# Optimization experiments

Hardware: AMD Instinct MI355X
Metric: run time of the kernel (lower is better)

Reference implementation:

```python
import jax, jax.numpy as jnp
import numpy as np

B, T, D, H = 8, 1024, 512, 8
HD = D // H  # head_dim = 64


def conv1d(x, w, b):
    # x: [B, C_in, T], w: [C_out, C_in, 3], 'same' padding
    y = jax.lax.conv_general_dilated(x, w, (1,), [(1, 1)],
                                     dimension_numbers=('NCH', 'OIH', 'NCH'))
    return y + b[None, :, None]


def setup_inputs() -> dict:
    key = jax.random.key(0)
    ks = jax.random.split(key, 9)
    s = 0.05
    return {
        'x': jax.random.normal(ks[0], (B, T, D), dtype=jnp.float32),
        'w11': jax.random.normal(ks[1], (D, D, 3), dtype=jnp.float32) * s,
        'b11': jnp.zeros((D,), dtype=jnp.float32),
        'w12': jax.random.normal(ks[2], (D, D, 3), dtype=jnp.float32) * s,
        'b12': jnp.zeros((D,), dtype=jnp.float32),
        'w13': jax.random.normal(ks[3], (D, D, 3), dtype=jnp.float32) * s,
        'b13': jnp.zeros((D,), dtype=jnp.float32),
        'w2': jax.random.normal(ks[4], (D, 2 * D, 3), dtype=jnp.float32) * s,
        'b2': jnp.zeros((D,), dtype=jnp.float32),
    }


def reference(x, w11, b11, w12, b12, w13, b13, w2, b2):
    # dropout is identity in eval mode
    b, t, d = x.shape
    xc = jnp.transpose(x, (0, 2, 1))  # [B, D, T]

    def proj(w, bb):
        y = jax.nn.relu(conv1d(xc, w, bb))        # [B, D, T]
        y = jnp.transpose(y, (0, 2, 1))           # [B, T, D]
        return y.reshape(b, t, H, HD)             # [B, T, H, HD]

    q = proj(w11, b11)
    k = proj(w12, b12)
    v = proj(w13, b13)

    # ---- time-wise attention (d_k = head_dim) ----
    qf = jnp.transpose(q, (0, 2, 1, 3))  # [B, H, T, HD]
    kf = jnp.transpose(k, (0, 2, 1, 3))
    vf = jnp.transpose(v, (0, 2, 1, 3))
    sf = jnp.einsum('bhtd,bhsd->bhts', qf, kf) / np.sqrt(HD)  # [B,H,T,T]
    af = jax.nn.softmax(sf, axis=-1)
    valuesf = jnp.einsum('bhts,bhsd->bhtd', af, vf)           # [B,H,T,HD]
    valuesf = jnp.transpose(valuesf, (0, 2, 1, 3)).reshape(b, t, H * HD)

    # ---- channel-wise attention (d_k = T, scores over head_dim) ----
    qt = jnp.transpose(q, (0, 2, 3, 1))  # [B, H, HD, T]
    kt = jnp.transpose(k, (0, 2, 3, 1))
    vt = jnp.transpose(v, (0, 2, 3, 1))
    st = jnp.einsum('bhct,bhdt->bhcd', qt, kt) / np.sqrt(t)   # [B,H,HD,HD]
    at = jax.nn.softmax(st, axis=-1)
    valuest = jnp.einsum('bhcd,bhdt->bhct', at, vt)           # [B,H,HD,T]
    # torch: permute(0,2,3,1).reshape(B, T, H*HD)
    valuest = jnp.transpose(valuest, (0, 2, 3, 1)).reshape(b, t, H * HD)

    values = jnp.concatenate([valuesf, valuest], axis=-1)     # [B, T, 2D]
    values = jnp.transpose(values, (0, 2, 1))                 # [B, 2D, T]
    out = jax.nn.relu(conv1d(values, w2, b2))                 # [B, D, T]
    return jnp.transpose(out, (0, 2, 1))                      # [B, T, D]
```

## Files before the change

kernel.cpp:

```cpp
#include <hip/hip_runtime.h>

#define BB 8
#define TT 1024
#define DD 512
#define DD2 1024
#define HH 8
#define HDIM 64
#define TP (TT + 2)

typedef short short8 __attribute__((ext_vector_type(8)));
typedef float floatx4 __attribute__((ext_vector_type(4)));

typedef const __attribute__((address_space(1))) unsigned int* gas_ptr;
typedef __attribute__((address_space(3))) unsigned int* las_ptr;

__device__ __forceinline__ unsigned short f2bf(float f) {
    union { float f; unsigned u; } v; v.f = f;
    unsigned r = v.u + 0x7fffu + ((v.u >> 16) & 1u);
    return (unsigned short)(r >> 16);
}

__device__ __forceinline__ void gl2lds16(const void* g, void* l) {
    __builtin_amdgcn_global_load_lds((gas_ptr)g, (las_ptr)l, 16, 0, 0);
}

__global__ void k_convert_x(const float* __restrict__ x, unsigned short* __restrict__ xp) {
    int idx = blockIdx.x * 256 + threadIdx.x;
    const int total = BB * TP * DD;
    if (idx >= total) return;
    int c = idx % DD;
    int rt = idx / DD;
    int row = rt % TP;
    int b = rt / TP;
    float v = 0.f;
    if (row >= 1 && row <= TT) v = x[(b * TT + row - 1) * DD + c];
    xp[idx] = f2bf(v);
}

__global__ void k_convert_wqkv(const float* __restrict__ w0, const float* __restrict__ w1,
                               const float* __restrict__ w2, unsigned short* __restrict__ out) {
    int idx = blockIdx.x * 256 + threadIdx.x;
    const int total = 9 << 18;
    if (idx >= total) return;
    int e = idx & 7;
    int lane = (idx >> 3) & 63;
    int co0 = (idx >> 9) & 31;
    int ci0 = (idx >> 14) & 15;
    int rest = idx >> 18;
    int k = rest % 3, p = rest / 3;
    int co = co0 * 16 + (lane & 15);
    int ci = ci0 * 32 + (lane >> 4) * 8 + e;
    const float* w = (p == 0) ? w0 : ((p == 1) ? w1 : w2);
    out[idx] = f2bf(w[(co * DD + ci) * 3 + k]);
}

__global__ void k_convert_w2(const float* __restrict__ w, unsigned short* __restrict__ out) {
    int idx = blockIdx.x * 256 + threadIdx.x;
    const int total = 3 << 19;
    if (idx >= total) return;
    int e = idx & 7;
    int lane = (idx >> 3) & 63;
    int co0 = (idx >> 9) & 31;
    int ci0 = (idx >> 14) & 31;
    int k = idx >> 19;
    int co = co0 * 16 + (lane & 15);
    int ci = ci0 * 32 + (lane >> 4) * 8 + e;
    out[idx] = f2bf(w[(co * DD2 + ci) * 3 + k]);
}

__global__ void k_zero_aux(unsigned short* __restrict__ vp, float* __restrict__ gbuf) {
    int idx = blockIdx.x * 256 + threadIdx.x;
    if (idx < BB * 2 * 2 * DD) {
        int c = idx % (2 * DD);
        int t1 = idx / (2 * DD);
        int row = (t1 & 1) ? (TT + 1) : 0;
        int b = t1 >> 1;
        vp[(b * TP + row) * (2 * DD) + c] = 0;
    }
    if (idx < 64 * HDIM * HDIM) gbuf[idx] = 0.f;
}

__global__ __launch_bounds__(256) void k_qkv_conv(
    const unsigned short* __restrict__ xp, const unsigned short* __restrict__ wfrag,
    const float* __restrict__ b11, const float* __restrict__ b12, const float* __restrict__ b13,
    unsigned short* __restrict__ q, unsigned short* __restrict__ qt,
    unsigned short* __restrict__ kfrag, unsigned short* __restrict__ kt,
    unsigned short* __restrict__ v, unsigned short* __restrict__ vtfrag) {
    __shared__ short As[2][144 * 32];
    int wave = threadIdx.x >> 6, lane = threadIdx.x & 63;
    int l15 = lane & 15, quad = lane >> 4;
    int wm = wave >> 1, wn = wave & 1;
    int tb = blockIdx.x * 128;
    int cb = blockIdx.y * 128;
    int proj = blockIdx.z % 3, b = blockIdx.z / 3;
    const short* A = (const short*)xp + b * TP * DD;
    const short* WF = (const short*)wfrag + (size_t)proj * 786432 + lane * 8;
    int srow = lane >> 2;
    int scs = (((lane & 3) ^ (srow & 3)) << 3);
    int co0b = (cb >> 4) + wn * 4;

    floatx4 acc[4][4];
#pragma unroll
    for (int mi = 0; mi < 4; ++mi)
#pragma unroll
        for (int ni = 0; ni < 4; ++ni) acc[mi][ni] = (floatx4){0.f, 0.f, 0.f, 0.f};

    for (int j = wave; j < 9; j += 4)
        gl2lds16(A + (tb + j * 16 + srow) * DD + scs, &As[0][j * 512]);
    __syncthreads();

    for (int it = 0; it < 16; ++it) {
        if (it < 15) {
            for (int j = wave; j < 9; j += 4)
                gl2lds16(A + (tb + j * 16 + srow) * DD + (it + 1) * 32 + scs,
                         &As[(it + 1) & 1][j * 512]);
        }
        const short* Asb = As[it & 1];
        short8 bf[3][4];
#pragma unroll
        for (int k = 0; k < 3; ++k)
#pragma unroll
            for (int ni = 0; ni < 4; ++ni)
                bf[k][ni] = *(const short8*)(WF + ((size_t)((k * 16 + it) * 32 + co0b + ni) << 9));
#pragma unroll
        for (int k = 0; k < 3; ++k) {
            short8 af[4];
#pragma unroll
            for (int mi = 0; mi < 4; ++mi) {
                int arow = wm * 64 + mi * 16 + l15 + k;
                af[mi] = *(const short8*)&Asb[arow * 32 + ((quad ^ (arow & 3)) << 3)];
            }
#pragma unroll
            for (int mi = 0; mi < 4; ++mi)
#pragma unroll
                for (int ni = 0; ni < 4; ++ni)
                    acc[mi][ni] = __builtin_amdgcn_mfma_f32_16x16x32_bf16(af[mi], bf[k][ni], acc[mi][ni], 0, 0, 0);
        }
        __syncthreads();
    }

    const float* bias = (proj == 0) ? b11 : ((proj == 1) ? b12 : b13);
#pragma unroll
    for (int ni = 0; ni < 4; ++ni) {
        int co = cb + wn * 64 + ni * 16 + l15;
        float bv = bias[co];
        int h = co >> 6, hd = co & 63;
        int bh = b * HH + h;
#pragma unroll
        for (int mi = 0; mi < 4; ++mi) {
            int tbase = tb + wm * 64 + mi * 16 + quad * 4;
            unsigned short bb[4];
            ushort4 pk;
#pragma unroll
            for (int r = 0; r < 4; ++r) {
                float val = fmaxf(acc[mi][ni][r] + bv, 0.f);
                bb[r] = f2bf(val);
                ((unsigned short*)&pk)[r] = bb[r];
            }
            if (proj == 0) {
#pragma unroll
                for (int r = 0; r < 4; ++r)
                    q[((size_t)bh * TT + tbase + r) * HDIM + hd] = bb[r];
                *(ushort4*)&qt[((size_t)bh * HDIM + hd) * TT + tbase] = pk;
            } else if (proj == 1) {
                *(ushort4*)&kt[((size_t)bh * HDIM + hd) * TT + tbase] = pk;
                int sblk = tbase >> 6;
                int jr = (quad & 1) + 2 * (mi >> 1);
                int l15a_base = 4 * (quad >> 1) + 8 * (mi & 1);
                int kf = hd >> 5, quad_a = (hd >> 3) & 3, elem = hd & 7;
                size_t base = ((((size_t)bh * 16 + sblk) * 4 + jr) * 2 + kf) * 512 +
                              quad_a * 128 + elem;
#pragma unroll
                for (int r = 0; r < 4; ++r)
                    kfrag[base + (l15a_base + r) * 8] = bb[r];
            } else {
#pragma unroll
                for (int r = 0; r < 4; ++r)
                    v[((size_t)bh * TT + tbase + r) * HDIM + hd] = bb[r];
                int sblk = tbase >> 6;
                int df = hd >> 4, l15a = hd & 15;
                int kf = mi >> 1;
                int quad_a = 2 * (mi & 1) + (quad >> 1);
                int elem = (quad & 1) * 4;
                size_t base = ((((size_t)bh * 16 + sblk) * 4 + df) * 2 + kf) * 512 +
                              (quad_a * 16 + l15a) * 8 + elem;
                *(ushort4*)&vtfrag[base] = pk;
            }
        }
    }
}

__global__ __launch_bounds__(256) void k_time_attn(
    const unsigned short* __restrict__ q, const unsigned short* __restrict__ kfrag,
    const unsigned short* __restrict__ vtfrag, unsigned short* __restrict__ vp) {
    int wave = threadIdx.x >> 6, lane = threadIdx.x & 63;
    int l15 = lane & 15, quad = lane >> 4;
    int bh = blockIdx.y;
    int b = bh >> 3, h = bh & 7;
    int qr = blockIdx.x * 64 + wave * 16;
    const short* Q = (const short*)q + (size_t)bh * TT * HDIM;
    const short* KF = (const short*)kfrag + (size_t)bh * 16 * 8 * 512 + lane * 8;
    const short* VF = (const short*)vtfrag + (size_t)bh * 16 * 8 * 512 + lane * 8;

    short8 bq[2];
#pragma unroll
    for (int kf = 0; kf < 2; ++kf)
        bq[kf] = *(const short8*)(Q + (qr + l15) * HDIM + kf * 32 + quad * 8);

    floatx4 o[4];
#pragma unroll
    for (int df = 0; df < 4; ++df) o[df] = (floatx4){0.f, 0.f, 0.f, 0.f};
    float lacc = 0.f;

    for (int sblk = 0; sblk < 16; ++sblk) {
        const short* kp = KF + sblk * 8 * 512;
        const short* vv = VF + sblk * 8 * 512;
        floatx4 c[4];
#pragma unroll
        for (int jr = 0; jr < 4; ++jr) c[jr] = (floatx4){0.f, 0.f, 0.f, 0.f};
#pragma unroll
        for (int jr = 0; jr < 4; ++jr) {
#pragma unroll
            for (int kf = 0; kf < 2; ++kf) {
                short8 ak = *(const short8*)(kp + (jr * 2 + kf) * 512);
                c[jr] = __builtin_amdgcn_mfma_f32_16x16x32_bf16(ak, bq[kf], c[jr], 0, 0, 0);
            }
        }
        short8 pb[2];
#pragma unroll
        for (int kf = 0; kf < 2; ++kf) {
            union { short8 s; unsigned u[4]; } pk;
#pragma unroll
            for (int half = 0; half < 2; ++half) {
                floatx4 cc = c[2 * kf + half];
                float p0 = __expf(cc[0] * 0.125f);
                float p1 = __expf(cc[1] * 0.125f);
                float p2 = __expf(cc[2] * 0.125f);
                float p3 = __expf(cc[3] * 0.125f);
                lacc += (p0 + p1) + (p2 + p3);
                pk.u[half * 2] =
                    __builtin_amdgcn_perm(__float_as_uint(p1), __float_as_uint(p0), 0x07060302u);
                pk.u[half * 2 + 1] =
                    __builtin_amdgcn_perm(__float_as_uint(p3), __float_as_uint(p2), 0x07060302u);
            }
            pb[kf] = pk.s;
        }
#pragma unroll
        for (int df = 0; df < 4; ++df) {
#pragma unroll
            for (int kf = 0; kf < 2; ++kf) {
                short8 av = *(const short8*)(vv + (df * 2 + kf) * 512);
                o[df] = __builtin_amdgcn_mfma_f32_16x16x32_bf16(av, pb[kf], o[df], 0, 0, 0);
            }
        }
    }

    lacc += __shfl_xor(lacc, 16);
    lacc += __shfl_xor(lacc, 32);
    float linv = 1.f / lacc;

    unsigned short* vrow = vp + (size_t)(b * TP + 1 + qr + l15) * (2 * DD) + h * 64;
#pragma unroll
    for (int df = 0; df < 4; ++df) {
        ushort4 pk;
#pragma unroll
        for (int r = 0; r < 4; ++r) ((unsigned short*)&pk)[r] = f2bf(o[df][r] * linv);
        *(ushort4*)&vrow[df * 16 + quad * 4] = pk;
    }
}

__global__ __launch_bounds__(256) void k_chan_gram(
    const unsigned short* __restrict__ qt, const unsigned short* __restrict__ kt,
    float* __restrict__ gbuf) {
    int wave = threadIdx.x >> 6, lane = threadIdx.x & 63;
    int l15 = lane & 15, quad = lane >> 4;
    int tc = blockIdx.x, bh = blockIdx.y;
    const short* Qt = (const short*)qt + (size_t)bh * HDIM * TT;
    const short* Kt = (const short*)kt + (size_t)bh * HDIM * TT;

    floatx4 g[4];
#pragma unroll
    for (int nt = 0; nt < 4; ++nt) g[nt] = (floatx4){0.f, 0.f, 0.f, 0.f};

    int t0b = tc * 256;
    for (int t0 = 0; t0 < 256; t0 += 32) {
        short8 aq = *(const short8*)(Qt + (wave * 16 + l15) * TT + t0b + t0 + quad * 8);
#pragma unroll
        for (int nt = 0; nt < 4; ++nt) {
            short8 bk = *(const short8*)(Kt + (nt * 16 + l15) * TT + t0b + t0 + quad * 8);
            g[nt] = __builtin_amdgcn_mfma_f32_16x16x32_bf16(aq, bk, g[nt], 0, 0, 0);
        }
    }
    float* gb = gbuf + bh * HDIM * HDIM;
#pragma unroll
    for (int nt = 0; nt < 4; ++nt) {
#pragma unroll
        for (int r = 0; r < 4; ++r) {
            int row = wave * 16 + quad * 4 + r;
            atomicAdd(&gb[row * HDIM + nt * 16 + l15], g[nt][r]);
        }
    }
}

__global__ __launch_bounds__(256) void k_chan_av(
    const float* __restrict__ gbuf, const unsigned short* __restrict__ v,
    unsigned short* __restrict__ vp) {
    __shared__ short lds_a[64 * 64];
    int wave = threadIdx.x >> 6, lane = threadIdx.x & 63;
    int l15 = lane & 15, quad = lane >> 4;
    int tc = blockIdx.x, bh = blockIdx.y;
    int b = bh >> 3, h = bh & 7;
    const float sc = 0.03125f;

    if (threadIdx.x < 64) {
        const float* gb = gbuf + bh * HDIM * HDIM + threadIdx.x * HDIM;
        float mx = -3.0e38f;
        for (int j = 0; j < 64; ++j) mx = fmaxf(mx, gb[j] * sc);
        float sum = 0.f;
        for (int j = 0; j < 64; ++j) sum += __expf(gb[j] * sc - mx);
        float inv = 1.f / sum;
        for (int j = 0; j < 64; ++j)
            lds_a[threadIdx.x * 64 + j] = (short)f2bf(__expf(gb[j] * sc - mx) * inv);
    }
    __syncthreads();

    const short* V = (const short*)v + (size_t)bh * TT * HDIM;
    short8 pa[2];
#pragma unroll
    for (int kf = 0; kf < 2; ++kf)
        pa[kf] = *(const short8*)&lds_a[(wave * 16 + l15) * 64 + kf * 32 + quad * 8];

    for (int tt = 0; tt < 16; ++tt) {
        int ttile = tc * 16 + tt;
        floatx4 c = (floatx4){0.f, 0.f, 0.f, 0.f};
#pragma unroll
        for (int kf = 0; kf < 2; ++kf) {
            short8 bv = *(const short8*)(V + (ttile * 16 + l15) * HDIM + kf * 32 + quad * 8);
            c = __builtin_amdgcn_mfma_f32_16x16x32_bf16(pa[kf], bv, c, 0, 0, 0);
        }
        int t = ttile * 16 + l15;
#pragma unroll
        for (int r = 0; r < 4; ++r) {
            int crow = wave * 16 + quad * 4 + r;
            int tout = crow * 16 + (t >> 6);
            int col = 512 + ((t & 63) << 3) + h;
            vp[(b * TP + 1 + tout) * (2 * DD) + col] = f2bf(c[r]);
        }
    }
}

__global__ __launch_bounds__(256) void k_out_conv(
    const unsigned short* __restrict__ vp, const unsigned short* __restrict__ w2k,
    const float* __restrict__ b2, float* __restrict__ out) {
    __shared__ short As[2][144 * 32];
    int wave = threadIdx.x >> 6, lane = threadIdx.x & 63;
    int l15 = lane & 15, quad = lane >> 4;
    int wm = wave >> 1, wn = wave & 1;
    int tb = blockIdx.x * 128;
    int cb = blockIdx.y * 64;
    int b = blockIdx.z;
    const short* A = (const short*)vp + b * TP * DD2;
    const short* WF = (const short*)w2k + lane * 8;
    int srow = lane >> 2;
    int scs = (((lane & 3) ^ (srow & 3)) << 3);
    int co0b = (cb >> 4) + wn * 2;

    floatx4 acc[4][2];
#pragma unroll
    for (int mi = 0; mi < 4; ++mi)
#pragma unroll
        for (int ni = 0; ni < 2; ++ni) acc[mi][ni] = (floatx4){0.f, 0.f, 0.f, 0.f};

    for (int j = wave; j < 9; j += 4)
        gl2lds16(A + (tb + j * 16 + srow) * DD2 + scs, &As[0][j * 512]);
    __syncthreads();

    for (int it = 0; it < 32; ++it) {
        if (it < 31) {
            for (int j = wave; j < 9; j += 4)
                gl2lds16(A + (tb + j * 16 + srow) * DD2 + (it + 1) * 32 + scs,
                         &As[(it + 1) & 1][j * 512]);
        }
        const short* Asb = As[it & 1];
        short8 bf[3][2];
#pragma unroll
        for (int k = 0; k < 3; ++k)
#pragma unroll
            for (int ni = 0; ni < 2; ++ni)
                bf[k][ni] = *(const short8*)(WF + ((size_t)((k * 32 + it) * 32 + co0b + ni) << 9));
#pragma unroll
        for (int k = 0; k < 3; ++k) {
            short8 af[4];
#pragma unroll
            for (int mi = 0; mi < 4; ++mi) {
                int arow = wm * 64 + mi * 16 + l15 + k;
                af[mi] = *(const short8*)&Asb[arow * 32 + ((quad ^ (arow & 3)) << 3)];
            }
#pragma unroll
            for (int mi = 0; mi < 4; ++mi)
#pragma unroll
                for (int ni = 0; ni < 2; ++ni)
                    acc[mi][ni] = __builtin_amdgcn_mfma_f32_16x16x32_bf16(af[mi], bf[k][ni], acc[mi][ni], 0, 0, 0);
        }
        __syncthreads();
    }

#pragma unroll
    for (int ni = 0; ni < 2; ++ni) {
        int co = cb + wn * 32 + ni * 16 + l15;
        float bv = b2[co];
#pragma unroll
        for (int mi = 0; mi < 4; ++mi) {
#pragma unroll
            for (int r = 0; r < 4; ++r) {
                int t = tb + wm * 64 + mi * 16 + quad * 4 + r;
                out[((size_t)b * TT + t) * DD + co] = fmaxf(acc[mi][ni][r] + bv, 0.f);
            }
        }
    }
}

extern "C" void kernel_launch(void* const* d_in, const int* in_sizes, int n_in,
                              void* d_out, int out_size, void* d_ws, size_t ws_size,
                              hipStream_t stream) {
    const float* x = (const float*)d_in[0];
    const float* w11 = (const float*)d_in[1];
    const float* b11 = (const float*)d_in[2];
    const float* w12 = (const float*)d_in[3];
    const float* b12 = (const float*)d_in[4];
    const float* w13 = (const float*)d_in[5];
    const float* b13 = (const float*)d_in[6];
    const float* w2 = (const float*)d_in[7];
    const float* b2 = (const float*)d_in[8];
    float* out = (float*)d_out;

    char* ws = (char*)d_ws;
    size_t off = 0;
    auto alloc = [&](size_t bytes) {
        void* p = ws + off;
        off += (bytes + 255) & ~(size_t)255;
        return p;
    };
    unsigned short* xp = (unsigned short*)alloc((size_t)BB * TP * DD * 2);
    unsigned short* wqkv = (unsigned short*)alloc((size_t)9 * DD * DD * 2);
    unsigned short* w2k = (unsigned short*)alloc((size_t)3 * DD * DD2 * 2);
    unsigned short* q = (unsigned short*)alloc((size_t)BB * HH * TT * HDIM * 2);
    unsigned short* qt = (unsigned short*)alloc((size_t)BB * HH * TT * HDIM * 2);
    unsigned short* kfrag = (unsigned short*)alloc((size_t)BB * HH * TT * HDIM * 2);
    unsigned short* kt = (unsigned short*)alloc((size_t)BB * HH * TT * HDIM * 2);
    unsigned short* v = (unsigned short*)alloc((size_t)BB * HH * TT * HDIM * 2);
    unsigned short* vtfrag = (unsigned short*)alloc((size_t)BB * HH * TT * HDIM * 2);
    float* gbuf = (float*)alloc((size_t)64 * HDIM * HDIM * 4);
    unsigned short* vp = (unsigned short*)alloc((size_t)BB * TP * 2 * DD * 2);
    (void)alloc(65536);

    k_convert_x<<<(BB * TP * DD + 255) / 256, 256, 0, stream>>>(x, xp);
    k_convert_wqkv<<<((9 << 18) + 255) / 256, 256, 0, stream>>>(w11, w12, w13, wqkv);
    k_convert_w2<<<((3 << 19) + 255) / 256, 256, 0, stream>>>(w2, w2k);
    k_zero_aux<<<(64 * HDIM * HDIM + 255) / 256, 256, 0, stream>>>(vp, gbuf);
    k_qkv_conv<<<dim3(TT / 128, DD / 128, BB * 3), 256, 0, stream>>>(xp, wqkv, b11, b12, b13,
                                                                     q, qt, kfrag, kt, v, vtfrag);
    k_time_attn<<<dim3(TT / 64, BB * HH), 256, 0, stream>>>(q, kfrag, vtfrag, vp);
    k_chan_gram<<<dim3(4, BB * HH), 256, 0, stream>>>(qt, kt, gbuf);
    k_chan_av<<<dim3(4, BB * HH), 256, 0, stream>>>(gbuf, v, vp);
    k_out_conv<<<dim3(TT / 128, DD / 64, BB), 256, 0, stream>>>(vp, w2k, b2, out);
}
```

Before: 264.0 us.

## Merge prep kernels into one launch and double K-tile depth in conv GEMMs

Combines the four input/weight conversion and zeroing kernels into one k_prep launch with block-range dispatch, removing three kernel launches. Both convolution GEMM kernels now stage 64-channel K slices into LDS instead of 32, using an 8-way XOR swizzle. This halves the number of main-loop iterations and barriers. The cost is doubled shared memory per block (about 36KB), which may lower occupancy.

```diff
diff --git a/kernel.cpp b/kernel.cpp
--- a/kernel.cpp
+++ b/kernel.cpp
@@ -24,60 +24,68 @@
     __builtin_amdgcn_global_load_lds((gas_ptr)g, (las_ptr)l, 16, 0, 0);
 }
 
-__global__ void k_convert_x(const float* __restrict__ x, unsigned short* __restrict__ xp) {
-    int idx = blockIdx.x * 256 + threadIdx.x;
-    const int total = BB * TP * DD;
-    if (idx >= total) return;
-    int c = idx % DD;
-    int rt = idx / DD;
-    int row = rt % TP;
-    int b = rt / TP;
-    float v = 0.f;
-    if (row >= 1 && row <= TT) v = x[(b * TT + row - 1) * DD + c];
-    xp[idx] = f2bf(v);
-}
-
-__global__ void k_convert_wqkv(const float* __restrict__ w0, const float* __restrict__ w1,
-                               const float* __restrict__ w2, unsigned short* __restrict__ out) {
-    int idx = blockIdx.x * 256 + threadIdx.x;
-    const int total = 9 << 18;
-    if (idx >= total) return;
-    int e = idx & 7;
-    int lane = (idx >> 3) & 63;
-    int co0 = (idx >> 9) & 31;
-    int ci0 = (idx >> 14) & 15;
-    int rest = idx >> 18;
-    int k = rest % 3, p = rest / 3;
-    int co = co0 * 16 + (lane & 15);
-    int ci = ci0 * 32 + (lane >> 4) * 8 + e;
-    const float* w = (p == 0) ? w0 : ((p == 1) ? w1 : w2);
-    out[idx] = f2bf(w[(co * DD + ci) * 3 + k]);
-}
-
-__global__ void k_convert_w2(const float* __restrict__ w, unsigned short* __restrict__ out) {
-    int idx = blockIdx.x * 256 + threadIdx.x;
-    const int total = 3 << 19;
-    if (idx >= total) return;
-    int e = idx & 7;
-    int lane = (idx >> 3) & 63;
-    int co0 = (idx >> 9) & 31;
-    int ci0 = (idx >> 14) & 31;
-    int k = idx >> 19;
-    int co = co0 * 16 + (lane & 15);
-    int ci = ci0 * 32 + (lane >> 4) * 8 + e;
-    out[idx] = f2bf(w[(co * DD2 + ci) * 3 + k]);
-}
-
-__global__ void k_zero_aux(unsigned short* __restrict__ vp, float* __restrict__ gbuf) {
-    int idx = blockIdx.x * 256 + threadIdx.x;
-    if (idx < BB * 2 * 2 * DD) {
-        int c = idx % (2 * DD);
-        int t1 = idx / (2 * DD);
-        int row = (t1 & 1) ? (TT + 1) : 0;
-        int b = t1 >> 1;
-        vp[(b * TP + row) * (2 * DD) + c] = 0;
-    }
-    if (idx < 64 * HDIM * HDIM) gbuf[idx] = 0.f;
+#define NXBLK 16416
+#define NW1BLK 9216
+#define NW2BLK 6144
+#define NZBLK 1024
+__global__ void k_prep(const float* __restrict__ x, const float* __restrict__ w0,
+                       const float* __restrict__ w1, const float* __restrict__ w2,
+                       const float* __restrict__ wo,
+                       unsigned short* __restrict__ xp, unsigned short* __restrict__ wqkv,
+                       unsigned short* __restrict__ w2k, unsigned short* __restrict__ vp,
+                       float* __restrict__ gbuf) {
+    int blk = blockIdx.x;
+    if (blk < NXBLK) {
+        int idx = blk * 256 + threadIdx.x;
+        int c = idx % DD;
+        int rt = idx / DD;
+        int row = rt % TP;
+        int b = rt / TP;
+        float v = 0.f;
+        if (row >= 1 && row <= TT) v = x[(b * TT + row - 1) * DD + c];
+        xp[idx] = f2bf(v);
+        return;
+    }
+    blk -= NXBLK;
+    if (blk < NW1BLK) {
+        int idx = blk * 256 + threadIdx.x;
+        int e = idx & 7;
+        int lane = (idx >> 3) & 63;
+        int co0 = (idx >> 9) & 31;
+        int ci0 = (idx >> 14) & 15;
+        int rest = idx >> 18;
+        int k = rest % 3, p = rest / 3;
+        int co = co0 * 16 + (lane & 15);
+        int ci = ci0 * 32 + (lane >> 4) * 8 + e;
+        const float* w = (p == 0) ? w0 : ((p == 1) ? w1 : w2);
+        wqkv[idx] = f2bf(w[(co * DD + ci) * 3 + k]);
+        return;
+    }
+    blk -= NW1BLK;
+    if (blk < NW2BLK) {
+        int idx = blk * 256 + threadIdx.x;
+        int e = idx & 7;
+        int lane = (idx >> 3) & 63;
+        int co0 = (idx >> 9) & 31;
+        int ci0 = (idx >> 14) & 31;
+        int k = idx >> 19;
+        int co = co0 * 16 + (lane & 15);
+        int ci = ci0 * 32 + (lane >> 4) * 8 + e;
+        w2k[idx] = f2bf(wo[(co * DD2 + ci) * 3 + k]);
+        return;
+    }
+    blk -= NW2BLK;
+    {
+        int idx = blk * 256 + threadIdx.x;
+        if (idx < BB * 2 * 2 * DD) {
+            int c = idx % (2 * DD);
+            int t1 = idx / (2 * DD);
+            int row = (t1 & 1) ? (TT + 1) : 0;
+            int b = t1 >> 1;
+            vp[(b * TP + row) * (2 * DD) + c] = 0;
+        }
+        if (idx < 64 * HDIM * HDIM) gbuf[idx] = 0.f;
+    }
 }
 
 __global__ __launch_bounds__(256) void k_qkv_conv(
@@ -86,7 +94,7 @@
     unsigned short* __restrict__ q, unsigned short* __restrict__ qt,
     unsigned short* __restrict__ kfrag, unsigned short* __restrict__ kt,
     unsigned short* __restrict__ v, unsigned short* __restrict__ vtfrag) {
-    __shared__ short As[2][144 * 32];
+    __shared__ short As[2][144 * 64];
     int wave = threadIdx.x >> 6, lane = threadIdx.x & 63;
     int l15 = lane & 15, quad = lane >> 4;
     int wm = wave >> 1, wn = wave & 1;
@@ -95,8 +103,8 @@
     int proj = blockIdx.z % 3, b = blockIdx.z / 3;
     const short* A = (const short*)xp + b * TP * DD;
     const short* WF = (const short*)wfrag + (size_t)proj * 786432 + lane * 8;
-    int srow = lane >> 2;
-    int scs = (((lane & 3) ^ (srow & 3)) << 3);
+    int srow8 = lane >> 3;
+    int scl = ((lane & 7) ^ srow8) * 8;
     int co0b = (cb >> 4) + wn * 4;
 
     floatx4 acc[4][4];
@@ -105,36 +113,46 @@
 #pragma unroll
         for (int ni = 0; ni < 4; ++ni) acc[mi][ni] = (floatx4){0.f, 0.f, 0.f, 0.f};
 
-    for (int j = wave; j < 9; j += 4)
-        gl2lds16(A + (tb + j * 16 + srow) * DD + scs, &As[0][j * 512]);
+    auto stage = [&](int it) {
+        short* dst = As[it & 1];
+        int cib = it * 64;
+        for (int g = wave; g < 18; g += 4) {
+            int j = g >> 1, hf = g & 1;
+            int row = hf * 8 + srow8;
+            gl2lds16(A + (tb + j * 16 + row) * DD + cib + scl, &dst[j * 1024 + hf * 512]);
+        }
+    };
+
+    stage(0);
     __syncthreads();
 
-    for (int it = 0; it < 16; ++it) {
-        if (it < 15) {
-            for (int j = wave; j < 9; j += 4)
-                gl2lds16(A + (tb + j * 16 + srow) * DD + (it + 1) * 32 + scs,
-                         &As[(it + 1) & 1][j * 512]);
-        }
+    for (int it = 0; it < 8; ++it) {
+        if (it < 7) stage(it + 1);
         const short* Asb = As[it & 1];
-        short8 bf[3][4];
-#pragma unroll
-        for (int k = 0; k < 3; ++k)
-#pragma unroll
-            for (int ni = 0; ni < 4; ++ni)
-                bf[k][ni] = *(const short8*)(WF + ((size_t)((k * 16 + it) * 32 + co0b + ni) << 9));
 #pragma unroll
         for (int k = 0; k < 3; ++k) {
-            short8 af[4];
-#pragma unroll
-            for (int mi = 0; mi < 4; ++mi) {
-                int arow = wm * 64 + mi * 16 + l15 + k;
-                af[mi] = *(const short8*)&Asb[arow * 32 + ((quad ^ (arow & 3)) << 3)];
-            }
-#pragma unroll
-            for (int mi = 0; mi < 4; ++mi)
+            short8 bf[2][4];
+#pragma unroll
+            for (int kfh = 0; kfh < 2; ++kfh)
 #pragma unroll
                 for (int ni = 0; ni < 4; ++ni)
-                    acc[mi][ni] = __builtin_amdgcn_mfma_f32_16x16x32_bf16(af[mi], bf[k][ni], acc[mi][ni], 0, 0, 0);
+                    bf[kfh][ni] = *(const short8*)(WF +
+                        ((size_t)((k * 16 + it * 2 + kfh) * 32 + co0b + ni) << 9));
+#pragma unroll
+            for (int kfh = 0; kfh < 2; ++kfh) {
+                short8 af[4];
+#pragma unroll
+                for (int mi = 0; mi < 4; ++mi) {
+                    int arow = wm * 64 + mi * 16 + l15 + k;
+                    int cl = kfh * 4 + quad;
+                    af[mi] = *(const short8*)&Asb[arow * 64 + ((cl ^ (arow & 7)) << 3)];
+                }
+#pragma unroll
+                for (int mi = 0; mi < 4; ++mi)
+#pragma unroll
+                    for (int ni = 0; ni < 4; ++ni)
+                        acc[mi][ni] = __builtin_amdgcn_mfma_f32_16x16x32_bf16(af[mi], bf[kfh][ni], acc[mi][ni], 0, 0, 0);
+            }
         }
         __syncthreads();
     }
@@ -352,7 +370,7 @@
 __global__ __launch_bounds__(256) void k_out_conv(
     const unsigned short* __restrict__ vp, const unsigned short* __restrict__ w2k,
     const float* __restrict__ b2, float* __restrict__ out) {
-    __shared__ short As[2][144 * 32];
+    __shared__ short As[2][144 * 64];
     int wave = threadIdx.x >> 6, lane = threadIdx.x & 63;
     int l15 = lane & 15, quad = lane >> 4;
     int wm = wave >> 1, wn = wave & 1;
@@ -361,8 +379,8 @@
     int b = blockIdx.z;
     const short* A = (const short*)vp + b * TP * DD2;
     const short* WF = (const short*)w2k + lane * 8;
-    int srow = lane >> 2;
-    int scs = (((lane & 3) ^ (srow & 3)) << 3);
+    int srow8 = lane >> 3;
+    int scl = ((lane & 7) ^ srow8) * 8;
     int co0b = (cb >> 4) + wn * 2;
 
     floatx4 acc[4][2];
@@ -371,36 +389,46 @@
 #pragma unroll
         for (int ni = 0; ni < 2; ++ni) acc[mi][ni] = (floatx4){0.f, 0.f, 0.f, 0.f};
 
-    for (int j = wave; j < 9; j += 4)
-        gl2lds16(A + (tb + j * 16 + srow) * DD2 + scs, &As[0][j * 512]);
+    auto stage = [&](int it) {
+        short* dst = As[it & 1];
+        int cib = it * 64;
+        for (int g = wave; g < 18; g += 4) {
+            int j = g >> 1, hf = g & 1;
+            int row = hf * 8 + srow8;
+            gl2lds16(A + (tb + j * 16 + row) * DD2 + cib + scl, &dst[j * 1024 + hf * 512]);
+        }
+    };
+
+    stage(0);
     __syncthreads();
 
-    for (int it = 0; it < 32; ++it) {
-        if (it < 31) {
-            for (int j = wave; j < 9; j += 4)
-                gl2lds16(A + (tb + j * 16 + srow) * DD2 + (it + 1) * 32 + scs,
-                         &As[(it + 1) & 1][j * 512]);
-        }
+    for (int it = 0; it < 16; ++it) {
+        if (it < 15) stage(it + 1);
         const short* Asb = As[it & 1];
-        short8 bf[3][2];
-#pragma unroll
-        for (int k = 0; k < 3; ++k)
-#pragma unroll
-            for (int ni = 0; ni < 2; ++ni)
-                bf[k][ni] = *(const short8*)(WF + ((size_t)((k * 32 + it) * 32 + co0b + ni) << 9));
 #pragma unroll
         for (int k = 0; k < 3; ++k) {
-            short8 af[4];
-#pragma unroll
-            for (int mi = 0; mi < 4; ++mi) {
-                int arow = wm * 64 + mi * 16 + l15 + k;
-                af[mi] = *(const short8*)&Asb[arow * 32 + ((quad ^ (arow & 3)) << 3)];
-            }
-#pragma unroll
-            for (int mi = 0; mi < 4; ++mi)
+            short8 bf[2][2];
+#pragma unroll
+            for (int kfh = 0; kfh < 2; ++kfh)
 #pragma unroll
                 for (int ni = 0; ni < 2; ++ni)
-                    acc[mi][ni] = __builtin_amdgcn_mfma_f32_16x16x32_bf16(af[mi], bf[k][ni], acc[mi][ni], 0, 0, 0);
+                    bf[kfh][ni] = *(const short8*)(WF +
+                        ((size_t)((k * 32 + it * 2 + kfh) * 32 + co0b + ni) << 9));
+#pragma unroll
+            for (int kfh = 0; kfh < 2; ++kfh) {
+                short8 af[4];
+#pragma unroll
+                for (int mi = 0; mi < 4; ++mi) {
+                    int arow = wm * 64 + mi * 16 + l15 + k;
+                    int cl = kfh * 4 + quad;
+                    af[mi] = *(const short8*)&Asb[arow * 64 + ((cl ^ (arow & 7)) << 3)];
+                }
+#pragma unroll
+                for (int mi = 0; mi < 4; ++mi)
+#pragma unroll
+                    for (int ni = 0; ni < 2; ++ni)
+                        acc[mi][ni] = __builtin_amdgcn_mfma_f32_16x16x32_bf16(af[mi], bf[kfh][ni], acc[mi][ni], 0, 0, 0);
+            }
         }
         __syncthreads();
     }
@@ -454,10 +482,8 @@
     unsigned short* vp = (unsigned short*)alloc((size_t)BB * TP * 2 * DD * 2);
     (void)alloc(65536);
 
-    k_convert_x<<<(BB * TP * DD + 255) / 256, 256, 0, stream>>>(x, xp);
-    k_convert_wqkv<<<((9 << 18) + 255) / 256, 256, 0, stream>>>(w11, w12, w13, wqkv);
-    k_convert_w2<<<((3 << 19) + 255) / 256, 256, 0, stream>>>(w2, w2k);
-    k_zero_aux<<<(64 * HDIM * HDIM + 255) / 256, 256, 0, stream>>>(vp, gbuf);
+    k_prep<<<NXBLK + NW1BLK + NW2BLK + NZBLK, 256, 0, stream>>>(x, w11, w12, w13, w2,
+                                                                xp, wqkv, w2k, vp, gbuf);
     k_qkv_conv<<<dim3(TT / 128, DD / 128, BB * 3), 256, 0, stream>>>(xp, wqkv, b11, b12, b13,
                                                                      q, qt, kfrag, kt, v, vtfrag);
     k_time_attn<<<dim3(TT / 64, BB * HH), 256, 0, stream>>>(q, kfrag, vtfrag, vp);
```

After: 246.3 us. -6.7%, faster.
